# Performance work log

Hardware: AMD Instinct MI355X
Metric: run time of the kernel (lower is better)

## Reference

```python
import jax, jax.numpy as jnp
import numpy as np

N_NODES = 10000
DEG = 32            # max_edges (fixed degree after padding)
CHANNELS = 16
IN_DIM = 4
BATCH = 8


def setup_inputs() -> dict:
    key = jax.random.key(0)
    k1, k2, k3 = jax.random.split(key, 3)
    E = N_NODES * DEG
    x = jax.random.normal(k1, (BATCH, N_NODES, IN_DIM), dtype=jnp.float32)
    # neighbor indices in [0, N_NODES]; index N_NODES is the padded 'useless' zero node
    edges = jax.random.randint(k2, (E,), 0, N_NODES + 1, dtype=jnp.int64)
    # torch.rand init: uniform [0,1); one weight tensor per input channel
    weights = jax.random.uniform(k3, (IN_DIM, E, CHANNELS), dtype=jnp.float32)
    return {"x": x, "edges": edges, "weights": weights}


def reference(x, edges, weights):
    B, N, in_dim = x.shape
    E = edges.shape[0]
    deg = E // N
    C = weights.shape[-1]
    # append zero 'useless node' so padding index N gathers zeros
    x_pad = jnp.concatenate([x, jnp.zeros((B, 1, in_dim), dtype=x.dtype)], axis=1)  # [B, N+1, in_dim]
    # super_edges = cat([edges]*C); viewed as [E, C] row-major (matches torch .view)
    idx = jnp.tile(edges, C).reshape(E, C)  # [E, C]
    out = jnp.zeros((B, N, C), dtype=x.dtype)
    for i in range(in_dim):  # small fixed loop over input channels (distinct weights)
        g = x_pad[:, :, i]              # [B, N+1]
        toc = g[:, idx]                 # gather -> [B, E, C]
        conv = toc * weights[i]         # per-edge weights broadcast over batch
        out = out + conv.reshape(B, N, deg, C).sum(axis=2)  # fixed-window segment sum
    return out
```

## Files before the change

### kernel.cpp

```cpp
#include <hip/hip_runtime.h>
#include <hip/hip_bf16.h>

#define N_NODES 10000
#define DEG     32
#define CH      16
#define IN_DIM  4
#define BATCH   8
#define E_EDGES (N_NODES * DEG)
#define WI_STRIDE (E_EDGES * CH)
#define P_COUNT 625
#define LX_STRIDE 36

__global__ __launch_bounds__(256) void lcg_transpose(const float* __restrict__ x,
                                                     float* __restrict__ xt) {
    int t = blockIdx.x * 256 + threadIdx.x;
    if (t < BATCH * N_NODES) {
        int b = t / N_NODES;
        int node = t - b * N_NODES;
        float4 v = *(const float4*)(x + 4 * t);
        *(float4*)(xt + node * 32 + b * 4) = v;
    } else if (t < BATCH * N_NODES + 8) {
        int r = t - BATCH * N_NODES;
        *(float4*)(xt + N_NODES * 32 + r * 4) = make_float4(0.f, 0.f, 0.f, 0.f);
    }
}

__global__ __launch_bounds__(256, 2) void lcg_main(
    const float* __restrict__ xt,
    const int*   __restrict__ edges,
    const float* __restrict__ w,
    float*       __restrict__ out)
{
    __shared__ float lx[512 * LX_STRIDE];

    int p = blockIdx.x;
    int t = threadIdx.x;

    {
        int sub = t & 7;
        int rg  = t >> 3;
        const int* ep = edges + 512 * p;
        int nd[16];
#pragma unroll
        for (int k = 0; k < 16; k++) nd[k] = ep[rg + 32 * k];
#pragma unroll
        for (int k = 0; k < 16; k++) {
            int s = rg + 32 * k;
            float4 v = *(const float4*)(xt + nd[k] * 32 + sub * 4);
            *(float4*)(&lx[s * LX_STRIDE + sub * 4]) = v;
        }
    }
    __syncthreads();

    int cq = t & 3;
    int j  = (t >> 2) & 15;
    int bq = t >> 6;
    int n  = p + P_COUNT * j;

    const float* wb = w + n * (DEG * CH) + 4 * cq;
    float accA[4] = {0.f, 0.f, 0.f, 0.f};
    float accB[4] = {0.f, 0.f, 0.f, 0.f};

#pragma unroll 2
    for (int d = 0; d < DEG; d++) {
        float4 w0 = *(const float4*)(wb + d * CH);
        float4 w1 = *(const float4*)(wb + d * CH + WI_STRIDE);
        float4 w2 = *(const float4*)(wb + d * CH + 2 * WI_STRIDE);
        float4 w3 = *(const float4*)(wb + d * CH + 3 * WI_STRIDE);
        const float* lrow = &lx[(16 * d + 4 * cq) * LX_STRIDE + 8 * bq];

#define CC_STEP(cc, s0, s1, s2, s3)                                         \
        {                                                                   \
            float4 xa = *(const float4*)(lrow + (cc) * LX_STRIDE);          \
            float4 xb = *(const float4*)(lrow + (cc) * LX_STRIDE + 4);      \
            accA[cc] += xa.x * (s0) + xa.y * (s1) + xa.z * (s2) + xa.w * (s3); \
            accB[cc] += xb.x * (s0) + xb.y * (s1) + xb.z * (s2) + xb.w * (s3); \
        }
        CC_STEP(0, w0.x, w1.x, w2.x, w3.x)
        CC_STEP(1, w0.y, w1.y, w2.y, w3.y)
        CC_STEP(2, w0.z, w1.z, w2.z, w3.z)
        CC_STEP(3, w0.w, w1.w, w2.w, w3.w)
#undef CC_STEP
    }

    int ob = n * CH + 4 * cq;
    *(float4*)(out + (2 * bq + 0) * (N_NODES * CH) + ob) =
        make_float4(accA[0], accA[1], accA[2], accA[3]);
    *(float4*)(out + (2 * bq + 1) * (N_NODES * CH) + ob) =
        make_float4(accB[0], accB[1], accB[2], accB[3]);
}

extern "C" void kernel_launch(void* const* d_in, const int* in_sizes, int n_in,
                              void* d_out, int out_size, void* d_ws, size_t ws_size,
                              hipStream_t stream) {
    const float* x     = (const float*)d_in[0];
    const int*   edges = (const int*)d_in[1];
    const float* w     = (const float*)d_in[2];
    float* out = (float*)d_out;
    float* xt  = (float*)d_ws;

    int tr_total  = BATCH * N_NODES + 8;
    int tr_blocks = (tr_total + 255) / 256;
    lcg_transpose<<<tr_blocks, 256, 0, stream>>>(x, xt);

    lcg_main<<<P_COUNT, 256, 0, stream>>>(xt, edges, w, out);
}
```

Before: 141.2 us.

## Split degree dimension across two blocks with partial buffers and add kernel

The main kernel now splits each block's 32-edge degree range into two halves handled by separate blocks. This doubles the grid to 1250 blocks and halves shared memory per block, allowing four blocks per CU instead of two. Each half writes a partial sum to a workspace buffer, and a new elementwise kernel adds the two partials into the output. The weight loads are also software-prefetched one iteration ahead. The cost is extra partial-buffer traffic (two 5 MB writes plus reads) and a third kernel launch.

```diff
diff --git a/kernel.cpp b/kernel.cpp
--- a/kernel.cpp
+++ b/kernel.cpp
@@ -10,6 +10,11 @@
 #define WI_STRIDE (E_EDGES * CH)
 #define P_COUNT 625
 #define LX_STRIDE 36
+#define OUT_FLOATS (BATCH * N_NODES * CH)
+
+#define WS_XT 0
+#define WS_P0 (2 * 1024 * 1024 / 4)
+#define WS_P1 (8 * 1024 * 1024 / 4)
 
 __global__ __launch_bounds__(256) void lcg_transpose(const float* __restrict__ x,
                                                      float* __restrict__ xt) {
@@ -25,29 +30,32 @@
     }
 }
 
-__global__ __launch_bounds__(256, 2) void lcg_main(
+__global__ __launch_bounds__(256, 4) void lcg_main(
     const float* __restrict__ xt,
     const int*   __restrict__ edges,
     const float* __restrict__ w,
-    float*       __restrict__ out)
+    float*       __restrict__ p0,
+    float*       __restrict__ p1)
 {
-    __shared__ float lx[512 * LX_STRIDE];
+    __shared__ float lx[256 * LX_STRIDE];
 
-    int p = blockIdx.x;
-    int t = threadIdx.x;
+    int bid = blockIdx.x;
+    int p  = bid >> 1;
+    int dh = bid & 1;
+    int t  = threadIdx.x;
 
     {
         int sub = t & 7;
         int rg  = t >> 3;
-        const int* ep = edges + 512 * p;
-        int nd[16];
+        const int* ep = edges + 512 * p + 256 * dh;
+        int nd[8];
 #pragma unroll
-        for (int k = 0; k < 16; k++) nd[k] = ep[rg + 32 * k];
+        for (int k = 0; k < 8; k++) nd[k] = ep[rg + 32 * k];
 #pragma unroll
-        for (int k = 0; k < 16; k++) {
-            int s = rg + 32 * k;
+        for (int k = 0; k < 8; k++) {
+            int r = rg + 32 * k;
             float4 v = *(const float4*)(xt + nd[k] * 32 + sub * 4);
-            *(float4*)(&lx[s * LX_STRIDE + sub * 4]) = v;
+            *(float4*)(&lx[r * LX_STRIDE + sub * 4]) = v;
         }
     }
     __syncthreads();
@@ -57,37 +65,53 @@
     int bq = t >> 6;
     int n  = p + P_COUNT * j;
 
-    const float* wb = w + n * (DEG * CH) + 4 * cq;
+    const float* wb = w + n * (DEG * CH) + 256 * dh + 4 * cq;
     float accA[4] = {0.f, 0.f, 0.f, 0.f};
     float accB[4] = {0.f, 0.f, 0.f, 0.f};
 
+    float4 wc0 = *(const float4*)(wb);
+    float4 wc1 = *(const float4*)(wb + WI_STRIDE);
+    float4 wc2 = *(const float4*)(wb + 2 * WI_STRIDE);
+    float4 wc3 = *(const float4*)(wb + 3 * WI_STRIDE);
+
 #pragma unroll 2
-    for (int d = 0; d < DEG; d++) {
-        float4 w0 = *(const float4*)(wb + d * CH);
-        float4 w1 = *(const float4*)(wb + d * CH + WI_STRIDE);
-        float4 w2 = *(const float4*)(wb + d * CH + 2 * WI_STRIDE);
-        float4 w3 = *(const float4*)(wb + d * CH + 3 * WI_STRIDE);
-        const float* lrow = &lx[(16 * d + 4 * cq) * LX_STRIDE + 8 * bq];
+    for (int dl = 0; dl < 16; dl++) {
+        int dn = dl < 15 ? dl + 1 : 15;
+        float4 wn0 = *(const float4*)(wb + dn * CH);
+        float4 wn1 = *(const float4*)(wb + dn * CH + WI_STRIDE);
+        float4 wn2 = *(const float4*)(wb + dn * CH + 2 * WI_STRIDE);
+        float4 wn3 = *(const float4*)(wb + dn * CH + 3 * WI_STRIDE);
 
-#define CC_STEP(cc, s0, s1, s2, s3)                                         \
-        {                                                                   \
-            float4 xa = *(const float4*)(lrow + (cc) * LX_STRIDE);          \
-            float4 xb = *(const float4*)(lrow + (cc) * LX_STRIDE + 4);      \
+        const float* lrow = &lx[(16 * dl + 4 * cq) * LX_STRIDE + 8 * bq];
+#define CC_STEP(cc, s0, s1, s2, s3)                                            \
+        {                                                                      \
+            float4 xa = *(const float4*)(lrow + (cc) * LX_STRIDE);             \
+            float4 xb = *(const float4*)(lrow + (cc) * LX_STRIDE + 4);         \
             accA[cc] += xa.x * (s0) + xa.y * (s1) + xa.z * (s2) + xa.w * (s3); \
             accB[cc] += xb.x * (s0) + xb.y * (s1) + xb.z * (s2) + xb.w * (s3); \
         }
-        CC_STEP(0, w0.x, w1.x, w2.x, w3.x)
-        CC_STEP(1, w0.y, w1.y, w2.y, w3.y)
-        CC_STEP(2, w0.z, w1.z, w2.z, w3.z)
-        CC_STEP(3, w0.w, w1.w, w2.w, w3.w)
+        CC_STEP(0, wc0.x, wc1.x, wc2.x, wc3.x)
+        CC_STEP(1, wc0.y, wc1.y, wc2.y, wc3.y)
+        CC_STEP(2, wc0.z, wc1.z, wc2.z, wc3.z)
+        CC_STEP(3, wc0.w, wc1.w, wc2.w, wc3.w)
 #undef CC_STEP
+        wc0 = wn0; wc1 = wn1; wc2 = wn2; wc3 = wn3;
     }
 
+    float* po = dh ? p1 : p0;
     int ob = n * CH + 4 * cq;
-    *(float4*)(out + (2 * bq + 0) * (N_NODES * CH) + ob) =
+    *(float4*)(po + (2 * bq + 0) * (N_NODES * CH) + ob) =
         make_float4(accA[0], accA[1], accA[2], accA[3]);
-    *(float4*)(out + (2 * bq + 1) * (N_NODES * CH) + ob) =
+    *(float4*)(po + (2 * bq + 1) * (N_NODES * CH) + ob) =
         make_float4(accB[0], accB[1], accB[2], accB[3]);
+}
+
+__global__ __launch_bounds__(256) void lcg_add(const float4* __restrict__ p0,
+                                               const float4* __restrict__ p1,
+                                               float4* __restrict__ o) {
+    int t = blockIdx.x * 256 + threadIdx.x;
+    float4 a = p0[t], b = p1[t];
+    o[t] = make_float4(a.x + b.x, a.y + b.y, a.z + b.z, a.w + b.w);
 }
 
 extern "C" void kernel_launch(void* const* d_in, const int* in_sizes, int n_in,
@@ -97,11 +121,17 @@
     const int*   edges = (const int*)d_in[1];
     const float* w     = (const float*)d_in[2];
     float* out = (float*)d_out;
-    float* xt  = (float*)d_ws;
+    float* ws  = (float*)d_ws;
+    float* xt  = ws + WS_XT;
+    float* p0  = ws + WS_P0;
+    float* p1  = ws + WS_P1;
 
     int tr_total  = BATCH * N_NODES + 8;
     int tr_blocks = (tr_total + 255) / 256;
     lcg_transpose<<<tr_blocks, 256, 0, stream>>>(x, xt);
 
-    lcg_main<<<P_COUNT, 256, 0, stream>>>(xt, edges, w, out);
+    lcg_main<<<2 * P_COUNT, 256, 0, stream>>>(xt, edges, w, p0, p1);
+
+    lcg_add<<<(OUT_FLOATS / 4) / 256, 256, 0, stream>>>(
+        (const float4*)p0, (const float4*)p1, (float4*)out);
 }
```

New measurement: 146.0 us. 3.4% more time.
